# Optimization experiments

Measured on AMD Instinct MI355X. Metric: run time of the kernel, lower is better.

Reference implementation:

```python
import jax, jax.numpy as jnp
import numpy as np

ANNEALING_SCALE = 0.1
BS, NV, S, D, V = 2, 16, 1024, 768, 50257

def setup_inputs() -> dict:
    key = jax.random.key(0)
    k1, k2, k3, k4, k5 = jax.random.split(key, 5)
    return {
        "input_ids": jax.random.randint(k1, (BS, S), 0, V),
        "content": jax.random.normal(k2, (BS, NV, S, D), dtype=jnp.float32),
        "contextualization": jax.random.normal(k3, (BS, NV, S, S), dtype=jnp.float32) * 0.05,
        "lm_head_weight": jax.random.normal(k4, (V, D), dtype=jnp.float32) * 0.02,
        "content_weights": jax.random.uniform(k5, (V, NV), dtype=jnp.float32),
    }

def reference(input_ids, content, contextualization, lm_head_weight, content_weights):
    bs, nv, s, d = content.shape
    # --- mask_annealing ---
    # Original computes relu(content @ W.T) over full vocab then gathers at input_ids.
    # Equivalent: gather rows of W first, then contract (same math since relu is
    # elementwise and only gathered columns are summed).
    Wg = lm_head_weight[input_ids]                              # (bs, s, d)
    sims = jnp.einsum('bkid,bjd->bkij', content, Wg)            # (bs, 16, s, s)
    sims = jnp.sum(jax.nn.relu(sims), axis=3)                   # (bs, 16, s)
    scores = jax.nn.sigmoid(-ANNEALING_SCALE * sims + 6.0)
    # upweight_nearby modifier
    scores = scores * (1.0 + jnp.arange(s, dtype=content.dtype) / 100.0)[None, None, :]
    scores = jnp.transpose(scores, (0, 2, 1))                   # (bs, s, 16)
    # --- create_content_soft_mask ---
    cw = content_weights[input_ids]                             # (bs, s, 16)
    weights = cw * scores + (1.0 - scores)                      # (bs, s, 16)
    # --- weighted sense combination ---
    content_m = content * jnp.transpose(weights, (0, 2, 1))[..., None]  # (bs,16,s,d)
    hidden = jnp.einsum('bkij,bkjd->bid', contextualization, content_m) # (bs, s, d)
    logits = hidden @ lm_head_weight.T                          # (bs, s, vocab)
    return logits
```

## Files before the change

### kernel.cpp

```cpp
#include <hip/hip_runtime.h>
#include <cstdint>
#include <cstddef>

#define BSZ 2
#define NV 16
#define SEQ 1024
#define DIM 768
#define VOC 50257
#define VOCP 50304

typedef unsigned int u32;
typedef unsigned short u16;
typedef _Float16 half8 __attribute__((ext_vector_type(8)));
typedef float f32x4 __attribute__((ext_vector_type(4)));

__device__ __forceinline__ u16 f2h(float f) {
  return __builtin_bit_cast(unsigned short, (_Float16)f);
}
__device__ __forceinline__ u32 pk2h(float a, float b) {
  return (u32)f2h(a) | ((u32)f2h(b) << 16);
}

__device__ __forceinline__ void gload16(const u16* g, u16* l) {
  __builtin_amdgcn_global_load_lds(
      (const __attribute__((address_space(1))) void*)g,
      (__attribute__((address_space(3))) void*)l, 16, 0, 0);
}

__global__ void k_prep_content(const float* __restrict__ content,
                               u16* __restrict__ cbf, u16* __restrict__ cT) {
  __shared__ u16 tile[32][33];
  const int bk = blockIdx.z;
  const int d0 = blockIdx.x * 32, j0 = blockIdx.y * 32;
  const float* src = content + (size_t)bk * SEQ * DIM;
  u16* dst = cbf + (size_t)bk * SEQ * DIM;
  u16* dstT = cT + (size_t)bk * DIM * SEQ;
  const int c = threadIdx.x;
#pragma unroll
  for (int rr = 0; rr < 4; ++rr) {
    const int r = threadIdx.y * 4 + rr;
    const float v = src[(size_t)(j0 + r) * DIM + d0 + c];
    const u16 bv = f2h(v);
    dst[(size_t)(j0 + r) * DIM + d0 + c] = bv;
    tile[r][c] = bv;
  }
  __syncthreads();
#pragma unroll
  for (int rr = 0; rr < 4; ++rr) {
    const int r = threadIdx.y * 4 + rr;
    dstT[(size_t)(d0 + r) * SEQ + j0 + c] = tile[c][r];
  }
}

__global__ void k_prep_w(const float* __restrict__ W, u16* __restrict__ Wb) {
  const int v = blockIdx.x;
  const int c = threadIdx.x * 4;
  u32 lo, hi;
  if (v < VOC) {
    const float4 f = *(const float4*)(W + (size_t)v * DIM + c);
    lo = pk2h(f.x, f.y); hi = pk2h(f.z, f.w);
  } else {
    lo = 0u; hi = 0u;
  }
  *(uint2*)(Wb + (size_t)v * DIM + c) = make_uint2(lo, hi);
}

__global__ void k_gather(const int* __restrict__ ids, const u16* __restrict__ Wb,
                         u16* __restrict__ Wg) {
  const int b = blockIdx.y, j = blockIdx.x;
  const int row = ids[b * SEQ + j];
  const int c = threadIdx.x * 4;
  *(uint2*)(Wg + ((size_t)b * SEQ + j) * DIM + c) =
      *(const uint2*)(Wb + (size_t)row * DIM + c);
}

__global__ void k_zero(float* __restrict__ p, int n) {
  const int i = blockIdx.x * 256 + threadIdx.x;
  if (i < n) p[i] = 0.f;
}

template <int LDA, int LDB>
__device__ __forceinline__ void gemm_core(const u16* __restrict__ A,
                                          const u16* __restrict__ B, int ksteps,
                                          u16* As, u16* Bs, f32x4 (&acc)[4][4],
                                          int t) {
  const int lane = t & 63, w = t >> 6, wr = w >> 1, wc = w & 1;
  const int rl = lane & 15;
  const int gsw = (((lane >> 4) ^ ((rl >> 1) & 3)) * 8);
  const int srow = 16 * w + (lane >> 2);
  const int sg = (((lane & 3) ^ ((lane >> 3) & 3)) * 8);
  const size_t gaBase = (size_t)srow * LDA + sg;
  const size_t gbBase = (size_t)srow * LDB + sg;
  u16* lA = As + w * 512;
  u16* lB = Bs + w * 512;

#define STAGE_(bb, kt)                                                  \
  {                                                                     \
    const u16* ga_ = A + gaBase + (size_t)(kt) * 32;                    \
    const u16* gb_ = B + gbBase + (size_t)(kt) * 32;                    \
    gload16(ga_, lA + (bb) * 4096);                                     \
    gload16(ga_ + (size_t)64 * LDA, lA + (bb) * 4096 + 2048);           \
    gload16(gb_, lB + (bb) * 4096);                                     \
    gload16(gb_ + (size_t)64 * LDB, lB + (bb) * 4096 + 2048);           \
  }

#define FRAGS_(bb)                                                      \
  half8 af[4], bf[4];                                                   \
  _Pragma("unroll") for (int m = 0; m < 4; ++m)                         \
      af[m] = *(const half8*)(As + (bb) * 4096 +                        \
                              (wr * 64 + m * 16 + rl) * 32 + gsw);      \
  _Pragma("unroll") for (int n = 0; n < 4; ++n)                         \
      bf[n] = *(const half8*)(Bs + (bb) * 4096 +                        \
                              (wc * 64 + n * 16 + rl) * 32 + gsw);      \
  _Pragma("unroll") for (int m = 0; m < 4; ++m)                         \
      _Pragma("unroll") for (int n = 0; n < 4; ++n)                     \
          acc[m][n] = __builtin_amdgcn_mfma_f32_16x16x32_f16(           \
              af[m], bf[n], acc[m][n], 0, 0, 0);

  STAGE_(0, 0);
  __syncthreads();
  int cur = 0;
  for (int kt = 0; kt < ksteps - 1; ++kt) {
    STAGE_(cur ^ 1, kt + 1);
    { FRAGS_(cur); }
    __syncthreads();
    cur ^= 1;
  }
  { FRAGS_(cur); }
#undef STAGE_
#undef FRAGS_
}

template <int LDA, int LDB>
__device__ __forceinline__ void gemm_core2(const u16* __restrict__ A0,
                                           const u16* __restrict__ A1,
                                           const u16* __restrict__ B, int ksteps,
                                           u16* As0, u16* As1, u16* Bs,
                                           f32x4 (&acc0)[4][4],
                                           f32x4 (&acc1)[4][4], int t) {
  const int lane = t & 63, w = t >> 6, wr = w >> 1, wc = w & 1;
  const int rl = lane & 15;
  const int gsw = (((lane >> 4) ^ ((rl >> 1) & 3)) * 8);
  const int srow = 16 * w + (lane >> 2);
  const int sg = (((lane & 3) ^ ((lane >> 3) & 3)) * 8);
  const size_t gaBase = (size_t)srow * LDA + sg;
  const size_t gbBase = (size_t)srow * LDB + sg;
  u16* lA0 = As0 + w * 512;
  u16* lA1 = As1 + w * 512;
  u16* lB = Bs + w * 512;

#define STAGE2_(bb, kt)                                                 \
  {                                                                     \
    const u16* ga0_ = A0 + gaBase + (size_t)(kt) * 32;                  \
    const u16* ga1_ = A1 + gaBase + (size_t)(kt) * 32;                  \
    const u16* gb_ = B + gbBase + (size_t)(kt) * 32;                    \
    gload16(ga0_, lA0 + (bb) * 4096);                                   \
    gload16(ga0_ + (size_t)64 * LDA, lA0 + (bb) * 4096 + 2048);         \
    gload16(ga1_, lA1 + (bb) * 4096);                                   \
    gload16(ga1_ + (size_t)64 * LDA, lA1 + (bb) * 4096 + 2048);         \
    gload16(gb_, lB + (bb) * 4096);                                     \
    gload16(gb_ + (size_t)64 * LDB, lB + (bb) * 4096 + 2048);           \
  }

#define FRAGS2_(bb)                                                     \
  half8 af0[4], af1[4], bf[4];                                          \
  _Pragma("unroll") for (int n = 0; n < 4; ++n)                         \
      bf[n] = *(const half8*)(Bs + (bb) * 4096 +                        \
                              (wc * 64 + n * 16 + rl) * 32 + gsw);      \
  _Pragma("unroll") for (int m = 0; m < 4; ++m)                         \
      af0[m] = *(const half8*)(As0 + (bb) * 4096 +                      \
                               (wr * 64 + m * 16 + rl) * 32 + gsw);     \
  _Pragma("unroll") for (int m = 0; m < 4; ++m)                         \
      af1[m] = *(const half8*)(As1 + (bb) * 4096 +                      \
                               (wr * 64 + m * 16 + rl) * 32 + gsw);     \
  _Pragma("unroll") for (int m = 0; m < 4; ++m)                         \
      _Pragma("unroll") for (int n = 0; n < 4; ++n)                     \
          acc0[m][n] = __builtin_amdgcn_mfma_f32_16x16x32_f16(          \
              af0[m], bf[n], acc0[m][n], 0, 0, 0);                      \
  _Pragma("unroll") for (int m = 0; m < 4; ++m)                         \
      _Pragma("unroll") for (int n = 0; n < 4; ++n)                     \
          acc1[m][n] = __builtin_amdgcn_mfma_f32_16x16x32_f16(          \
              af1[m], bf[n], acc1[m][n], 0, 0, 0);

  STAGE2_(0, 0);
  __syncthreads();
  int cur = 0;
  for (int kt = 0; kt < ksteps - 1; ++kt) {
    STAGE2_(cur ^ 1, kt + 1);
    { FRAGS2_(cur); }
    __syncthreads();
    cur ^= 1;
  }
  { FRAGS2_(cur); }
#undef STAGE2_
#undef FRAGS2_
}

__global__ __launch_bounds__(256, 2) void k_sims(const u16* __restrict__ cbf,
                                                 const u16* __restrict__ Wg,
                                                 float* __restrict__ sims) {
  __shared__ __align__(16) u16 As0[2 * 128 * 32];
  __shared__ __align__(16) u16 As1[2 * 128 * 32];
  __shared__ __align__(16) u16 Bs[2 * 128 * 32];
  const int bk = blockIdx.z, b = bk >> 4;
  const int t = threadIdx.x;
  const int i0 = blockIdx.y * 256;
  const u16* A0 = cbf + (size_t)bk * SEQ * DIM + (size_t)i0 * DIM;
  const u16* A1 = A0 + (size_t)128 * DIM;
  const u16* B = Wg + (size_t)b * SEQ * DIM + (size_t)(blockIdx.x * 128) * DIM;
  f32x4 acc0[4][4] = {}, acc1[4][4] = {};
  gemm_core2<DIM, DIM>(A0, A1, B, DIM / 32, As0, As1, Bs, acc0, acc1, t);
  const int lane = t & 63, w = t >> 6, wr = w >> 1;
  const int rg = lane >> 4, cl = lane & 15;
#pragma unroll
  for (int m = 0; m < 4; ++m) {
#pragma unroll
    for (int r = 0; r < 4; ++r) {
      float s0 = 0.f, s1 = 0.f;
#pragma unroll
      for (int n = 0; n < 4; ++n) {
        s0 += fmaxf(acc0[m][n][r], 0.f);
        s1 += fmaxf(acc1[m][n][r], 0.f);
      }
      s0 += __shfl_xor(s0, 1); s1 += __shfl_xor(s1, 1);
      s0 += __shfl_xor(s0, 2); s1 += __shfl_xor(s1, 2);
      s0 += __shfl_xor(s0, 4); s1 += __shfl_xor(s1, 4);
      s0 += __shfl_xor(s0, 8); s1 += __shfl_xor(s1, 8);
      if (cl == 0) {
        const int i = i0 + wr * 64 + m * 16 + rg * 4 + r;
        atomicAdd(&sims[(size_t)bk * SEQ + i], s0);
        atomicAdd(&sims[(size_t)bk * SEQ + i + 128], s1);
      }
    }
  }
}

__global__ void k_weights(const float* __restrict__ sims, const int* __restrict__ ids,
                          const float* __restrict__ cw, float* __restrict__ wtsT) {
  const int j = blockIdx.x * 256 + threadIdx.x;
  const int bk = blockIdx.y;
  const int b = bk >> 4, k = bk & 15;
  const float sm = sims[(size_t)bk * SEQ + j];
  float score = 1.f / (1.f + __expf(0.1f * sm - 6.f));
  score *= 1.f + (float)j * 0.01f;
  const int id = ids[b * SEQ + j];
  const float c = cw[(size_t)id * NV + k];
  wtsT[(size_t)bk * SEQ + j] = c * score + (1.f - score);
}

__global__ void k_ctx(const float* __restrict__ ctx, const float* __restrict__ wtsT,
                      u16* __restrict__ ctxw) {
  const size_t i = ((size_t)blockIdx.x * 256 + threadIdx.x) * 4;
  const float4 c = *(const float4*)(ctx + i);
  const size_t bk = i >> 20;
  const int j = (int)(i & (SEQ - 1));
  const float4 wv = *(const float4*)(wtsT + bk * SEQ + j);
  *(uint2*)(ctxw + i) =
      make_uint2(pk2h(c.x * wv.x, c.y * wv.y), pk2h(c.z * wv.z, c.w * wv.w));
}

__global__ __launch_bounds__(256) void k_hidden(const u16* __restrict__ ctxw,
                                                const u16* __restrict__ cT,
                                                float* __restrict__ part) {
  __shared__ __align__(16) u16 As[2 * 128 * 32];
  __shared__ __align__(16) u16 Bs[2 * 128 * 32];
  const int z = blockIdx.z;
  const int b = z >> 2, g = z & 3;
  const int i0 = blockIdx.y * 128, d0 = blockIdx.x * 128;
  const int t = threadIdx.x;
  f32x4 acc[4][4] = {};
  for (int kk = 0; kk < 4; ++kk) {
    const int sense = g * 4 + kk;
    const u16* A = ctxw + ((size_t)(b * NV + sense) * SEQ + i0) * SEQ;
    const u16* B = cT + ((size_t)(b * NV + sense) * DIM + d0) * SEQ;
    gemm_core<SEQ, SEQ>(A, B, SEQ / 32, As, Bs, acc, t);
    __syncthreads();
  }
  const int lane = t & 63, w = t >> 6, wr = w >> 1, wc = w & 1;
  const int rg = lane >> 4, cl = lane & 15;
  float* P = part + ((size_t)(g * BSZ + b) * SEQ + i0) * DIM + d0;
#pragma unroll
  for (int m = 0; m < 4; ++m)
#pragma unroll
    for (int n = 0; n < 4; ++n)
#pragma unroll
      for (int r = 0; r < 4; ++r)
        P[(size_t)(wr * 64 + m * 16 + rg * 4 + r) * DIM + wc * 64 + n * 16 + cl] =
            acc[m][n][r];
}

__global__ void k_reduce(const float* __restrict__ part, u16* __restrict__ hid) {
  const size_t i = ((size_t)blockIdx.x * 256 + threadIdx.x) * 4;
  const size_t NHID = (size_t)BSZ * SEQ * DIM;
  float4 s = {0.f, 0.f, 0.f, 0.f};
#pragma unroll
  for (int g = 0; g < 4; ++g) {
    const float4 p = *(const float4*)(part + (size_t)g * NHID + i);
    s.x += p.x; s.y += p.y; s.z += p.z; s.w += p.w;
  }
  *(uint2*)(hid + i) = make_uint2(pk2h(s.x, s.y), pk2h(s.z, s.w));
}

__global__ __launch_bounds__(256, 2) void k_logits(const u16* __restrict__ hid,
                                                   const u16* __restrict__ Wb,
                                                   float* __restrict__ out) {
  __shared__ __align__(16) u16 As0[2 * 128 * 32];
  __shared__ __align__(16) u16 As1[2 * 128 * 32];
  __shared__ __align__(16) u16 Bs[2 * 128 * 32];
  const int bid = blockIdx.x;
  const int swz = (bid & 7) * 393 + (bid >> 3);
  const int it = swz & 7, vt = swz >> 3;
  const int i0 = it * 256, v0 = vt * 128;
  const int t = threadIdx.x;
  const u16* A0 = hid + (size_t)i0 * DIM;
  const u16* A1 = A0 + (size_t)128 * DIM;
  const u16* B = Wb + (size_t)v0 * DIM;
  f32x4 acc0[4][4] = {}, acc1[4][4] = {};
  gemm_core2<DIM, DIM>(A0, A1, B, DIM / 32, As0, As1, Bs, acc0, acc1, t);
  const int lane = t & 63, w = t >> 6, wr = w >> 1, wc = w & 1;
  const int rg = lane >> 4, cl = lane & 15;
#pragma unroll
  for (int m = 0; m < 4; ++m)
#pragma unroll
    for (int n = 0; n < 4; ++n) {
      const int vv = v0 + wc * 64 + n * 16 + cl;
      if (vv < VOC) {
        const int i = i0 + wr * 64 + m * 16 + rg * 4;
#pragma unroll
        for (int r = 0; r < 4; ++r)
          out[(size_t)(i + r) * VOC + vv] = acc0[m][n][r];
#pragma unroll
        for (int r = 0; r < 4; ++r)
          out[(size_t)(i + 128 + r) * VOC + vv] = acc1[m][n][r];
      }
    }
}

extern "C" void kernel_launch(void* const* d_in, const int* in_sizes, int n_in,
                              void* d_out, int out_size, void* d_ws, size_t ws_size,
                              hipStream_t stream) {
  const int* ids = (const int*)d_in[0];
  const float* content = (const float*)d_in[1];
  const float* ctx = (const float*)d_in[2];
  const float* W = (const float*)d_in[3];
  const float* cw = (const float*)d_in[4];
  float* out = (float*)d_out;
  char* ws = (char*)d_ws;

  u16* cbf  = (u16*)(ws);
  u16* cT   = (u16*)(ws + 50331648);
  u16* Wb   = (u16*)(ws + 100663296);
  u16* Wg   = (u16*)(ws + 177930240);
  u16* ctxw = (u16*)(ws + 181075968);
  float* sims = (float*)(ws + 248184832);
  float* wtsT = (float*)(ws + 248315904);
  float* part = (float*)cbf;
  u16* hid = Wg;

  k_prep_content<<<dim3(DIM / 32, SEQ / 32, BSZ * NV), dim3(32, 8), 0, stream>>>(
      content, cbf, cT);
  k_prep_w<<<VOCP, 192, 0, stream>>>(W, Wb);
  k_gather<<<dim3(SEQ, BSZ), 192, 0, stream>>>(ids, Wb, Wg);
  k_zero<<<128, 256, 0, stream>>>(sims, BSZ * NV * SEQ);
  k_sims<<<dim3(8, 4, BSZ * NV), 256, 0, stream>>>(cbf, Wg, sims);
  k_weights<<<dim3(4, BSZ * NV), 256, 0, stream>>>(sims, ids, cw, wtsT);
  k_ctx<<<32768, 256, 0, stream>>>(ctx, wtsT, ctxw);
  k_hidden<<<dim3(6, 8, 8), 256, 0, stream>>>(ctxw, cT, part);
  k_reduce<<<1536, 256, 0, stream>>>(part, hid);
  k_logits<<<8 * 393, 256, 0, stream>>>(hid, Wb, out);
}
```

Baseline: 639.2 us.

## Triple-buffer LDS ring with explicit vmcnt waits in dual-tile GEMM core

```diff
diff --git a/kernel.cpp b/kernel.cpp
--- a/kernel.cpp
+++ b/kernel.cpp
@@ -132,7 +132,7 @@
 }
 
 template <int LDA, int LDB>
-__device__ __forceinline__ void gemm_core2(const u16* __restrict__ A0,
+__device__ __forceinline__ void gemm_ring2(const u16* __restrict__ A0,
                                            const u16* __restrict__ A1,
                                            const u16* __restrict__ B, int ksteps,
                                            u16* As0, u16* As1, u16* Bs,
@@ -145,34 +145,35 @@
   const int sg = (((lane & 3) ^ ((lane >> 3) & 3)) * 8);
   const size_t gaBase = (size_t)srow * LDA + sg;
   const size_t gbBase = (size_t)srow * LDB + sg;
-  u16* lA0 = As0 + w * 512;
-  u16* lA1 = As1 + w * 512;
-  u16* lB = Bs + w * 512;
-
-#define STAGE2_(bb, kt)                                                 \
+  const int wof = w * 512;
+
+#define STG3_(ss, kt)                                                   \
   {                                                                     \
     const u16* ga0_ = A0 + gaBase + (size_t)(kt) * 32;                  \
     const u16* ga1_ = A1 + gaBase + (size_t)(kt) * 32;                  \
     const u16* gb_ = B + gbBase + (size_t)(kt) * 32;                    \
-    gload16(ga0_, lA0 + (bb) * 4096);                                   \
-    gload16(ga0_ + (size_t)64 * LDA, lA0 + (bb) * 4096 + 2048);         \
-    gload16(ga1_, lA1 + (bb) * 4096);                                   \
-    gload16(ga1_ + (size_t)64 * LDA, lA1 + (bb) * 4096 + 2048);         \
-    gload16(gb_, lB + (bb) * 4096);                                     \
-    gload16(gb_ + (size_t)64 * LDB, lB + (bb) * 4096 + 2048);           \
-  }
-
-#define FRAGS2_(bb)                                                     \
+    gload16(ga0_, As0 + (ss) * 4096 + wof);                             \
+    gload16(ga0_ + (size_t)64 * LDA, As0 + (ss) * 4096 + wof + 2048);   \
+    gload16(ga1_, As1 + (ss) * 4096 + wof);                            \
+    gload16(ga1_ + (size_t)64 * LDA, As1 + (ss) * 4096 + wof + 2048);   \
+    gload16(gb_, Bs + (ss) * 4096 + wof);                              \
+    gload16(gb_ + (size_t)64 * LDB, Bs + (ss) * 4096 + wof + 2048);     \
+  }
+
+#define FRAGS3_(ss)                                                     \
   half8 af0[4], af1[4], bf[4];                                          \
   _Pragma("unroll") for (int n = 0; n < 4; ++n)                         \
-      bf[n] = *(const half8*)(Bs + (bb) * 4096 +                        \
+      bf[n] = *(const half8*)(Bs + (ss) * 4096 +                        \
                               (wc * 64 + n * 16 + rl) * 32 + gsw);      \
   _Pragma("unroll") for (int m = 0; m < 4; ++m)                         \
-      af0[m] = *(const half8*)(As0 + (bb) * 4096 +                      \
+      af0[m] = *(const half8*)(As0 + (ss) * 4096 +                      \
                                (wr * 64 + m * 16 + rl) * 32 + gsw);     \
   _Pragma("unroll") for (int m = 0; m < 4; ++m)                         \
-      af1[m] = *(const half8*)(As1 + (bb) * 4096 +                      \
-                               (wr * 64 + m * 16 + rl) * 32 + gsw);     \
+      af1[m] = *(const half8*)(As1 + (ss) * 4096 +                      \
+                               (wr * 64 + m * 16 + rl) * 32 + gsw);
+
+#define MFMA32_                                                         \
+  __builtin_amdgcn_s_setprio(1);                                        \
   _Pragma("unroll") for (int m = 0; m < 4; ++m)                         \
       _Pragma("unroll") for (int n = 0; n < 4; ++n)                     \
           acc0[m][n] = __builtin_amdgcn_mfma_f32_16x16x32_f16(          \
@@ -180,28 +181,54 @@
   _Pragma("unroll") for (int m = 0; m < 4; ++m)                         \
       _Pragma("unroll") for (int n = 0; n < 4; ++n)                     \
           acc1[m][n] = __builtin_amdgcn_mfma_f32_16x16x32_f16(          \
-              af1[m], bf[n], acc1[m][n], 0, 0, 0);
-
-  STAGE2_(0, 0);
-  __syncthreads();
-  int cur = 0;
-  for (int kt = 0; kt < ksteps - 1; ++kt) {
-    STAGE2_(cur ^ 1, kt + 1);
-    { FRAGS2_(cur); }
-    __syncthreads();
-    cur ^= 1;
-  }
-  { FRAGS2_(cur); }
-#undef STAGE2_
-#undef FRAGS2_
+              af1[m], bf[n], acc1[m][n], 0, 0, 0);                      \
+  __builtin_amdgcn_s_setprio(0);
+
+#define STEPF_(ss, kt)                                                  \
+  asm volatile("s_waitcnt vmcnt(6)" ::: "memory");                      \
+  __builtin_amdgcn_s_barrier();                                         \
+  __builtin_amdgcn_sched_barrier(0);                                    \
+  STG3_(((ss) + 2) % 3, (kt) + 2);                                      \
+  { FRAGS3_(ss) MFMA32_ }
+
+#define STEPL6_(ss)                                                     \
+  asm volatile("s_waitcnt vmcnt(6)" ::: "memory");                      \
+  __builtin_amdgcn_s_barrier();                                         \
+  __builtin_amdgcn_sched_barrier(0);                                    \
+  { FRAGS3_(ss) MFMA32_ }
+
+#define STEPL0_(ss)                                                     \
+  asm volatile("s_waitcnt vmcnt(0)" ::: "memory");                      \
+  __builtin_amdgcn_s_barrier();                                         \
+  __builtin_amdgcn_sched_barrier(0);                                    \
+  { FRAGS3_(ss) MFMA32_ }
+
+  STG3_(0, 0);
+  STG3_(1, 1);
+  const int nTrip = ksteps / 3;
+  for (int u = 0; u < nTrip - 1; ++u) {
+    const int kt = 3 * u;
+    STEPF_(0, kt);
+    STEPF_(1, kt + 1);
+    STEPF_(2, kt + 2);
+  }
+  STEPF_(0, ksteps - 3);
+  STEPL6_(1);
+  STEPL0_(2);
+#undef STG3_
+#undef FRAGS3_
+#undef MFMA32_
+#undef STEPF_
+#undef STEPL6_
+#undef STEPL0_
 }
 
 __global__ __launch_bounds__(256, 2) void k_sims(const u16* __restrict__ cbf,
                                                  const u16* __restrict__ Wg,
                                                  float* __restrict__ sims) {
-  __shared__ __align__(16) u16 As0[2 * 128 * 32];
-  __shared__ __align__(16) u16 As1[2 * 128 * 32];
-  __shared__ __align__(16) u16 Bs[2 * 128 * 32];
+  __shared__ __align__(16) u16 As0[3 * 4096];
+  __shared__ __align__(16) u16 As1[3 * 4096];
+  __shared__ __align__(16) u16 Bs[3 * 4096];
   const int bk = blockIdx.z, b = bk >> 4;
   const int t = threadIdx.x;
   const int i0 = blockIdx.y * 256;
@@ -209,7 +236,7 @@
   const u16* A1 = A0 + (size_t)128 * DIM;
   const u16* B = Wg + (size_t)b * SEQ * DIM + (size_t)(blockIdx.x * 128) * DIM;
   f32x4 acc0[4][4] = {}, acc1[4][4] = {};
-  gemm_core2<DIM, DIM>(A0, A1, B, DIM / 32, As0, As1, Bs, acc0, acc1, t);
+  gemm_ring2<DIM, DIM>(A0, A1, B, DIM / 32, As0, As1, Bs, acc0, acc1, t);
   const int lane = t & 63, w = t >> 6, wr = w >> 1;
   const int rg = lane >> 4, cl = lane & 15;
 #pragma unroll
@@ -304,9 +331,9 @@
 __global__ __launch_bounds__(256, 2) void k_logits(const u16* __restrict__ hid,
                                                    const u16* __restrict__ Wb,
                                                    float* __restrict__ out) {
-  __shared__ __align__(16) u16 As0[2 * 128 * 32];
-  __shared__ __align__(16) u16 As1[2 * 128 * 32];
-  __shared__ __align__(16) u16 Bs[2 * 128 * 32];
+  __shared__ __align__(16) u16 As0[3 * 4096];
+  __shared__ __align__(16) u16 As1[3 * 4096];
+  __shared__ __align__(16) u16 Bs[3 * 4096];
   const int bid = blockIdx.x;
   const int swz = (bid & 7) * 393 + (bid >> 3);
   const int it = swz & 7, vt = swz >> 3;
@@ -316,7 +343,7 @@
   const u16* A1 = A0 + (size_t)128 * DIM;
   const u16* B = Wb + (size_t)v0 * DIM;
   f32x4 acc0[4][4] = {}, acc1[4][4] = {};
-  gemm_core2<DIM, DIM>(A0, A1, B, DIM / 32, As0, As1, Bs, acc0, acc1, t);
+  gemm_ring2<DIM, DIM>(A0, A1, B, DIM / 32, As0, As1, Bs, acc0, acc1, t);
   const int lane = t & 63, w = t >> 6, wr = w >> 1, wc = w & 1;
   const int rg = lane >> 4, cl = lane & 15;
 #pragma unroll
```

New measurement: 591.4 us. -7.5%, faster.
